# Kernel optimization log

Hardware: AMD Instinct MI355X
Metric: run time of the kernel (lower is better)

Reference implementation:

```python
import jax, jax.numpy as jnp
import numpy as np

N_NODES = 100000
N_EDGES = 1280000
IN_C = 64
HID_C = 64
OUT_C = 64


def _sage_conv(x, src, dst, W_l, b_l, W_r, num_nodes):
    """PyG SAGEConv with mean aggregation:
    out = lin_l(mean_{j in N(i)} x_j) + lin_r(x_i)
    lin_l has bias, lin_r (root) has no bias."""
    msg = x[src]  # [E, C] gather of source-node features
    summed = jax.ops.segment_sum(msg, dst, num_segments=num_nodes)  # [N, C]
    cnt = jax.ops.segment_sum(jnp.ones((src.shape[0], 1), x.dtype), dst,
                              num_segments=num_nodes)  # [N, 1]
    agg = summed / jnp.maximum(cnt, 1)  # mean; isolated nodes -> 0
    return agg @ W_l.T + b_l + x @ W_r.T


def setup_inputs() -> dict:
    key = jax.random.key(0)
    ks = jax.random.split(key, 8)
    x = jax.random.normal(ks[0], (N_NODES, IN_C), dtype=jnp.float32)
    edge_index = jax.random.randint(ks[1], (2, N_EDGES), 0, N_NODES, dtype=jnp.int64)
    s1 = 1.0 / np.sqrt(IN_C)
    s2 = 1.0 / np.sqrt(HID_C)
    W1_l = jax.random.uniform(ks[2], (HID_C, IN_C), jnp.float32, -s1, s1)
    b1 = jax.random.uniform(ks[3], (HID_C,), jnp.float32, -s1, s1)
    W1_r = jax.random.uniform(ks[4], (HID_C, IN_C), jnp.float32, -s1, s1)
    W2_l = jax.random.uniform(ks[5], (OUT_C, HID_C), jnp.float32, -s2, s2)
    b2 = jax.random.uniform(ks[6], (OUT_C,), jnp.float32, -s2, s2)
    W2_r = jax.random.uniform(ks[7], (OUT_C, HID_C), jnp.float32, -s2, s2)
    return {"x": x, "edge_index": edge_index, "W1_l": W1_l, "b1": b1,
            "W1_r": W1_r, "W2_l": W2_l, "b2": b2, "W2_r": W2_r}


def reference(x, edge_index, W1_l, b1, W1_r, W2_l, b2, W2_r):
    src, dst = edge_index[0], edge_index[1]
    h = _sage_conv(x, src, dst, W1_l, b1, W1_r, N_NODES)
    h = jax.nn.relu(h)
    out = _sage_conv(h, src, dst, W2_l, b2, W2_r, N_NODES)
    return out
```

## Files before the change

kernel.cpp:

```cpp
#include <hip/hip_runtime.h>

constexpr int N = 100000;
constexpr int E = 1280000;
constexpr int C = 64;
constexpr int NB = (N + 255) / 256;
constexpr int EPB = 4096;
constexpr int NBIN = (E + EPB - 1) / EPB;
constexpr int CAP = 4096;

typedef __attribute__((ext_vector_type(8))) short bf16x8;
typedef __attribute__((ext_vector_type(4))) float f32x4;

__device__ __forceinline__ unsigned bfr(float v) {
    unsigned u = __float_as_uint(v);
    return (u + 0x7fffu + ((u >> 16) & 1u)) >> 16;
}
__device__ __forceinline__ float bflo(unsigned w) { return __uint_as_float(w << 16); }
__device__ __forceinline__ float bfhi(unsigned w) { return __uint_as_float(w & 0xffff0000u); }

__global__ __launch_bounds__(256) void cast_k(const float* __restrict__ x,
                                              uint2* __restrict__ xb) {
    int i = blockIdx.x * 256 + threadIdx.x;
    if (i < N * 16) {
        float4 v = ((const float4*)x)[i];
        uint2 o;
        o.x = bfr(v.x) | (bfr(v.y) << 16);
        o.y = bfr(v.z) | (bfr(v.w) << 16);
        xb[i] = o;
    }
}

__global__ __launch_bounds__(256) void wcast_k(const float* __restrict__ Wl,
                                               const float* __restrict__ Wr,
                                               unsigned* __restrict__ Wb) {
    int u = blockIdx.x * 256 + threadIdx.x;
    if (u < 64 * 64) {
        int c = u >> 5;
        int p = u & 31;
        float2 l = *(const float2*)(Wl + c * 64 + p * 2);
        float2 r = *(const float2*)(Wr + c * 64 + p * 2);
        Wb[c * 64 + p]      = bfr(l.x) | (bfr(l.y) << 16);
        Wb[c * 64 + 32 + p] = bfr(r.x) | (bfr(r.y) << 16);
    }
}

__global__ __launch_bounds__(256) void chist_k(const int* __restrict__ dst,
                                               int* __restrict__ bcnt) {
    __shared__ int h[NB];
    int t = threadIdx.x;
    for (int i = t; i < NB; i += 256) h[i] = 0;
    __syncthreads();
    int e0 = blockIdx.x * EPB;
    int eEnd = min(e0 + EPB, E);
    for (int e = e0 + t; e < eEnd; e += 256) atomicAdd(&h[dst[e] >> 8], 1);
    __syncthreads();
    for (int i = t; i < NB; i += 256)
        if (h[i]) atomicAdd(&bcnt[i], h[i]);
}

__global__ __launch_bounds__(512) void scanB_k(const int* __restrict__ bcnt,
                                               int* __restrict__ bbase,
                                               int* __restrict__ gcur) {
    __shared__ int s[2][512];
    int t = threadIdx.x;
    int v = (t < NB) ? bcnt[t] : 0;
    s[0][t] = v;
    __syncthreads();
    int p = 0;
    for (int off = 1; off < 512; off <<= 1) {
        int a = s[p][t] + (t >= off ? s[p][t - off] : 0);
        s[p ^ 1][t] = a;
        p ^= 1;
        __syncthreads();
    }
    if (t < NB) { bbase[t] = s[p][t] - v; gcur[t] = 0; }
}

__global__ __launch_bounds__(256) void bin_k(const int* __restrict__ src,
                                             const int* __restrict__ dst,
                                             const int* __restrict__ bbase,
                                             int* __restrict__ gcur,
                                             unsigned* __restrict__ tmp) {
    __shared__ int hist[NB];
    __shared__ int start[NB];
    __shared__ int cnt2[NB];
    __shared__ int gbase[NB];
    __shared__ unsigned pk[EPB];
    __shared__ unsigned short bkt[EPB];
    __shared__ int sc[2][512];
    int t = threadIdx.x;
    for (int i = t; i < NB; i += 256) { hist[i] = 0; cnt2[i] = 0; }
    __syncthreads();
    int e0 = blockIdx.x * EPB;
    int eEnd = min(e0 + EPB, E);
    for (int e = e0 + t; e < eEnd; e += 256) atomicAdd(&hist[dst[e] >> 8], 1);
    __syncthreads();
    sc[0][t]       = (t < NB) ? hist[t] : 0;
    sc[0][t + 256] = (t + 256 < NB) ? hist[t + 256] : 0;
    __syncthreads();
    int p = 0;
    for (int off = 1; off < 512; off <<= 1) {
        int a = sc[p][t]       + (t >= off ? sc[p][t - off] : 0);
        int b = sc[p][t + 256] + sc[p][t + 256 - off];
        sc[p ^ 1][t] = a;
        sc[p ^ 1][t + 256] = b;
        p ^= 1;
        __syncthreads();
    }
    if (t < NB)       start[t]       = sc[p][t]       - hist[t];
    if (t + 256 < NB) start[t + 256] = sc[p][t + 256] - hist[t + 256];
    __syncthreads();
    for (int e = e0 + t; e < eEnd; e += 256) {
        int d = dst[e];
        int b = d >> 8;
        int pos = start[b] + atomicAdd(&cnt2[b], 1);
        pk[pos] = ((unsigned)src[e] << 8) | (unsigned)(d & 255);
        bkt[pos] = (unsigned short)b;
    }
    __syncthreads();
    for (int i = t; i < NB; i += 256)
        gbase[i] = hist[i] ? bbase[i] + atomicAdd(&gcur[i], hist[i]) : 0;
    __syncthreads();
    int n = eEnd - e0;
    for (int i = t; i < n; i += 256) {
        int b = bkt[i];
        tmp[gbase[b] + (i - start[b])] = pk[i];
    }
}

__global__ __launch_bounds__(256) void bsort_k(const unsigned* __restrict__ tmp,
                                               const int* __restrict__ bbase,
                                               const int* __restrict__ bcnt,
                                               int* __restrict__ rowp,
                                               int* __restrict__ deg,
                                               int* __restrict__ csr) {
    int b = blockIdx.x;
    int base = bbase[b];
    int count = bcnt[b];
    __shared__ int h[256], st[256], c2[256];
    __shared__ int sc[2][256];
    __shared__ unsigned srcA[CAP];
    int t = threadIdx.x;
    h[t] = 0; c2[t] = 0;
    __syncthreads();
    for (int i = t; i < count; i += 256) atomicAdd(&h[tmp[base + i] & 255u], 1);
    __syncthreads();
    sc[0][t] = h[t];
    __syncthreads();
    int p = 0;
    for (int off = 1; off < 256; off <<= 1) {
        int a = sc[p][t] + (t >= off ? sc[p][t - off] : 0);
        sc[p ^ 1][t] = a;
        p ^= 1;
        __syncthreads();
    }
    int excl = sc[p][t] - h[t];
    st[t] = excl;
    int node = b * 256 + t;
    if (node < N) { rowp[node] = base + excl; deg[node] = h[t]; }
    __syncthreads();
    for (int i = t; i < count; i += 256) {
        unsigned pr = tmp[base + i];
        int d = (int)(pr & 255u);
        int pos = st[d] + atomicAdd(&c2[d], 1);
        srcA[pos] = pr >> 8;
    }
    __syncthreads();
    for (int i = t; i < count; i += 256) csr[base + i] = (int)srcA[i];
}

__global__ __launch_bounds__(256) void agg_k(const int* __restrict__ csr,
                                             const int* __restrict__ rowp,
                                             const int* __restrict__ deg,
                                             const uint2* __restrict__ featb,
                                             uint2* __restrict__ aggb) {
    int node = blockIdx.x * 4 + (threadIdx.x >> 6);
    int lane = threadIdx.x & 63;
    int g = lane >> 4;
    int q = lane & 15;
    int start = rowp[node];
    int d = deg[node];
    float4 acc = make_float4(0.f, 0.f, 0.f, 0.f);
    int j = g;
    for (; j + 4 < d; j += 8) {
        int s0 = csr[start + j];
        int s1 = csr[start + j + 4];
        uint2 u0 = featb[(size_t)s0 * 16 + q];
        uint2 u1 = featb[(size_t)s1 * 16 + q];
        acc.x += bflo(u0.x) + bflo(u1.x);
        acc.y += bfhi(u0.x) + bfhi(u1.x);
        acc.z += bflo(u0.y) + bflo(u1.y);
        acc.w += bfhi(u0.y) + bfhi(u1.y);
    }
    for (; j < d; j += 4) {
        int s0 = csr[start + j];
        uint2 u0 = featb[(size_t)s0 * 16 + q];
        acc.x += bflo(u0.x); acc.y += bfhi(u0.x);
        acc.z += bflo(u0.y); acc.w += bfhi(u0.y);
    }
#pragma unroll
    for (int off = 16; off <= 32; off <<= 1) {
        acc.x += __shfl_xor(acc.x, off);
        acc.y += __shfl_xor(acc.y, off);
        acc.z += __shfl_xor(acc.z, off);
        acc.w += __shfl_xor(acc.w, off);
    }
    if (g == 0) {
        float inv = d > 0 ? 1.f / (float)d : 0.f;
        uint2 o;
        o.x = bfr(acc.x * inv) | (bfr(acc.y * inv) << 16);
        o.y = bfr(acc.z * inv) | (bfr(acc.w * inv) << 16);
        aggb[(size_t)node * 16 + q] = o;
    }
}

template <int RELU, int OBF>
__global__ __launch_bounds__(256) void combine_mfma_k(
    const unsigned short* __restrict__ Ab,
    const unsigned short* __restrict__ Xb,
    const unsigned short* __restrict__ Wb,
    const float* __restrict__ bias,
    float* __restrict__ outF, unsigned short* __restrict__ outB) {
    int wave = threadIdx.x >> 6;
    int lane = threadIdx.x & 63;
    int row0 = (blockIdx.x * 4 + wave) * 16;
    if (row0 >= N) return;
    int g = lane >> 4;
    int r = lane & 15;
    int node = row0 + r;

    const unsigned short* arow = Ab + (size_t)node * 64 + g * 8;
    const unsigned short* xrow = Xb + (size_t)node * 64 + g * 8;
    bf16x8 a[4];
    a[0] = *(const bf16x8*)(const void*)(arow);
    a[1] = *(const bf16x8*)(const void*)(arow + 32);
    a[2] = *(const bf16x8*)(const void*)(xrow);
    a[3] = *(const bf16x8*)(const void*)(xrow + 32);

#pragma unroll
    for (int ct = 0; ct < 4; ++ct) {
        int c = ct * 16 + r;
        const unsigned short* wrow = Wb + (size_t)c * 128 + g * 8;
        f32x4 acc = {0.f, 0.f, 0.f, 0.f};
#pragma unroll
        for (int kc = 0; kc < 4; ++kc) {
            bf16x8 b = *(const bf16x8*)(const void*)(wrow + kc * 32);
            acc = __builtin_amdgcn_mfma_f32_16x16x32_bf16(a[kc], b, acc, 0, 0, 0);
        }
        float bs = bias[c];
#pragma unroll
        for (int rr = 0; rr < 4; ++rr) {
            int orow = row0 + g * 4 + rr;
            float v = acc[rr] + bs;
            if (RELU) v = fmaxf(v, 0.f);
            if (OBF) {
                float v1 = __shfl_xor(v, 1);
                if ((lane & 1) == 0) {
                    unsigned u = bfr(v) | (bfr(v1) << 16);
                    *(unsigned*)(void*)(outB + (size_t)orow * 64 + c) = u;
                }
            } else {
                outF[(size_t)orow * 64 + c] = v;
            }
        }
    }
}

extern "C" void kernel_launch(void* const* d_in, const int* in_sizes, int n_in,
                              void* d_out, int out_size, void* d_ws, size_t ws_size,
                              hipStream_t stream) {
    const float* x   = (const float*)d_in[0];
    const int*   ei  = (const int*)d_in[1];
    const int*   srcI = ei;
    const int*   dstI = ei + E;
    const float* W1l = (const float*)d_in[2];
    const float* b1  = (const float*)d_in[3];
    const float* W1r = (const float*)d_in[4];
    const float* W2l = (const float*)d_in[5];
    const float* b2  = (const float*)d_in[6];
    const float* W2r = (const float*)d_in[7];
    float* out = (float*)d_out;

    int*            bcnt  = (int*)d_ws;
    int*            bbase = bcnt + 512;
    int*            gcur  = bbase + 512;
    int*            deg   = gcur + 512;
    int*            rowp  = deg + 102400;
    int*            csr   = rowp + 102400;
    unsigned short* aggb  = (unsigned short*)(csr + E);
    unsigned short* xb    = aggb + (size_t)N * 64;
    unsigned short* hb    = xb + (size_t)N * 64;
    unsigned*       Wb1   = (unsigned*)(hb + (size_t)N * 64);
    unsigned*       Wb2   = Wb1 + 64 * 64;
    unsigned*       tmp   = (unsigned*)aggb;

    hipMemsetAsync(bcnt, 0, 512 * sizeof(int), stream);

    cast_k<<<(N * 16 + 255) / 256, 256, 0, stream>>>(x, (uint2*)xb);
    wcast_k<<<16, 256, 0, stream>>>(W1l, W1r, Wb1);
    wcast_k<<<16, 256, 0, stream>>>(W2l, W2r, Wb2);
    chist_k<<<NBIN, 256, 0, stream>>>(dstI, bcnt);
    scanB_k<<<1, 512, 0, stream>>>(bcnt, bbase, gcur);
    bin_k<<<NBIN, 256, 0, stream>>>(srcI, dstI, bbase, gcur, tmp);
    bsort_k<<<NB, 256, 0, stream>>>(tmp, bbase, bcnt, rowp, deg, csr);

    const int nAggBlocks = N / 4;
    const int nMfmaBlocks = (N / 16 + 3) / 4;

    agg_k<<<nAggBlocks, 256, 0, stream>>>(csr, rowp, deg, (const uint2*)xb, (uint2*)aggb);
    combine_mfma_k<1, 1><<<nMfmaBlocks, 256, 0, stream>>>(
        aggb, xb, (const unsigned short*)Wb1, b1, nullptr, hb);

    agg_k<<<nAggBlocks, 256, 0, stream>>>(csr, rowp, deg, (const uint2*)hb, (uint2*)aggb);
    combine_mfma_k<0, 0><<<nMfmaBlocks, 256, 0, stream>>>(
        aggb, hb, (const unsigned short*)Wb2, b2, out, nullptr);
}
```

Baseline: 178.3 us.

## Restructure mean aggregation to one wave per node with shuffled neighbor indices

The aggregation kernel now assigns a full 64-lane wave to each node, with each lane owning one feature channel. Neighbor indices are loaded cooperatively once per 64-edge chunk and broadcast with shuffles, and eight gathers are issued per iteration for memory-level parallelism. A grid-stride loop over 2048 blocks replaces one block per four nodes, and the cross-group shuffle reduction is removed. The trade-off is that each lane now does 2-byte gathers instead of 8-byte ones, and an extra shuffle is needed to pack bf16 pairs on output.

```diff
diff --git a/kernel.cpp b/kernel.cpp
--- a/kernel.cpp
+++ b/kernel.cpp
@@ -17,6 +17,9 @@
 }
 __device__ __forceinline__ float bflo(unsigned w) { return __uint_as_float(w << 16); }
 __device__ __forceinline__ float bfhi(unsigned w) { return __uint_as_float(w & 0xffff0000u); }
+__device__ __forceinline__ float bfs(unsigned short u) {
+    return __uint_as_float(((unsigned)u) << 16);
+}
 
 __global__ __launch_bounds__(256) void cast_k(const float* __restrict__ x,
                                               uint2* __restrict__ xb) {
@@ -172,45 +175,51 @@
 __global__ __launch_bounds__(256) void agg_k(const int* __restrict__ csr,
                                              const int* __restrict__ rowp,
                                              const int* __restrict__ deg,
-                                             const uint2* __restrict__ featb,
-                                             uint2* __restrict__ aggb) {
-    int node = blockIdx.x * 4 + (threadIdx.x >> 6);
+                                             const unsigned short* __restrict__ featb,
+                                             unsigned* __restrict__ aggb) {
     int lane = threadIdx.x & 63;
-    int g = lane >> 4;
-    int q = lane & 15;
-    int start = rowp[node];
-    int d = deg[node];
-    float4 acc = make_float4(0.f, 0.f, 0.f, 0.f);
-    int j = g;
-    for (; j + 4 < d; j += 8) {
-        int s0 = csr[start + j];
-        int s1 = csr[start + j + 4];
-        uint2 u0 = featb[(size_t)s0 * 16 + q];
-        uint2 u1 = featb[(size_t)s1 * 16 + q];
-        acc.x += bflo(u0.x) + bflo(u1.x);
-        acc.y += bfhi(u0.x) + bfhi(u1.x);
-        acc.z += bflo(u0.y) + bflo(u1.y);
-        acc.w += bfhi(u0.y) + bfhi(u1.y);
-    }
-    for (; j < d; j += 4) {
-        int s0 = csr[start + j];
-        uint2 u0 = featb[(size_t)s0 * 16 + q];
-        acc.x += bflo(u0.x); acc.y += bfhi(u0.x);
-        acc.z += bflo(u0.y); acc.w += bfhi(u0.y);
-    }
-#pragma unroll
-    for (int off = 16; off <= 32; off <<= 1) {
-        acc.x += __shfl_xor(acc.x, off);
-        acc.y += __shfl_xor(acc.y, off);
-        acc.z += __shfl_xor(acc.z, off);
-        acc.w += __shfl_xor(acc.w, off);
-    }
-    if (g == 0) {
+    int wid = blockIdx.x * 4 + (threadIdx.x >> 6);
+    int nw = gridDim.x * 4;
+    for (int node = wid; node < N; node += nw) {
+        int start = rowp[node];
+        int d = deg[node];
+        float acc = 0.f;
+        for (int jb = 0; jb < d; jb += 64) {
+            int nb = min(64, d - jb);
+            int idxv = (jb + lane < d) ? csr[start + jb + lane] : 0;
+            int j = 0;
+            for (; j + 7 < nb; j += 8) {
+                int s0 = __shfl(idxv, j);
+                int s1 = __shfl(idxv, j + 1);
+                int s2 = __shfl(idxv, j + 2);
+                int s3 = __shfl(idxv, j + 3);
+                int s4 = __shfl(idxv, j + 4);
+                int s5 = __shfl(idxv, j + 5);
+                int s6 = __shfl(idxv, j + 6);
+                int s7 = __shfl(idxv, j + 7);
+                unsigned short u0 = featb[((size_t)s0 << 6) + lane];
+                unsigned short u1 = featb[((size_t)s1 << 6) + lane];
+                unsigned short u2 = featb[((size_t)s2 << 6) + lane];
+                unsigned short u3 = featb[((size_t)s3 << 6) + lane];
+                unsigned short u4 = featb[((size_t)s4 << 6) + lane];
+                unsigned short u5 = featb[((size_t)s5 << 6) + lane];
+                unsigned short u6 = featb[((size_t)s6 << 6) + lane];
+                unsigned short u7 = featb[((size_t)s7 << 6) + lane];
+                acc += ((bfs(u0) + bfs(u1)) + (bfs(u2) + bfs(u3)))
+                     + ((bfs(u4) + bfs(u5)) + (bfs(u6) + bfs(u7)));
+            }
+            for (; j < nb; ++j) {
+                int s0 = __shfl(idxv, j);
+                acc += bfs(featb[((size_t)s0 << 6) + lane]);
+            }
+        }
         float inv = d > 0 ? 1.f / (float)d : 0.f;
-        uint2 o;
-        o.x = bfr(acc.x * inv) | (bfr(acc.y * inv) << 16);
-        o.y = bfr(acc.z * inv) | (bfr(acc.w * inv) << 16);
-        aggb[(size_t)node * 16 + q] = o;
+        float v = acc * inv;
+        float vn = __shfl_xor(v, 1);
+        if ((lane & 1) == 0) {
+            unsigned o = bfr(v) | (bfr(vn) << 16);
+            aggb[((size_t)node << 5) + (lane >> 1)] = o;
+        }
     }
 }
 
@@ -304,14 +313,14 @@
     bin_k<<<NBIN, 256, 0, stream>>>(srcI, dstI, bbase, gcur, tmp);
     bsort_k<<<NB, 256, 0, stream>>>(tmp, bbase, bcnt, rowp, deg, csr);
 
-    const int nAggBlocks = N / 4;
+    const int nAggBlocks = 2048;
     const int nMfmaBlocks = (N / 16 + 3) / 4;
 
-    agg_k<<<nAggBlocks, 256, 0, stream>>>(csr, rowp, deg, (const uint2*)xb, (uint2*)aggb);
+    agg_k<<<nAggBlocks, 256, 0, stream>>>(csr, rowp, deg, xb, (unsigned*)aggb);
     combine_mfma_k<1, 1><<<nMfmaBlocks, 256, 0, stream>>>(
         aggb, xb, (const unsigned short*)Wb1, b1, nullptr, hb);
 
-    agg_k<<<nAggBlocks, 256, 0, stream>>>(csr, rowp, deg, (const uint2*)hb, (uint2*)aggb);
+    agg_k<<<nAggBlocks, 256, 0, stream>>>(csr, rowp, deg, hb, (unsigned*)aggb);
     combine_mfma_k<0, 0><<<nMfmaBlocks, 256, 0, stream>>>(
         aggb, hb, (const unsigned short*)Wb2, b2, out, nullptr);
 }
```

After: 190.6 us. 1.07x slower.
